# Optimization experiments

Measured on AMD Instinct MI355X. Metric: run time of the kernel, lower is better.

## Reference

```python
import jax, jax.numpy as jnp
import numpy as np

B, T, I, H, L, O = 256, 256, 512, 1024, 2, 5


def setup_inputs() -> dict:
    key = jax.random.key(0)
    ks = jax.random.split(key, 8)
    x = jax.random.normal(ks[0], (B, T, I), dtype=jnp.float32)
    hidden = jnp.zeros((L, 2, B, H), dtype=jnp.float32)  # [layer, (h,c), B, H]
    # per-layer stacked gate weights: [4(gates f,i,g,o), H, in+H]
    W0 = jax.random.normal(ks[1], (4, H, I + H), dtype=jnp.float32) * 0.01
    b0 = jnp.zeros((4, H), dtype=jnp.float32)
    W1 = jax.random.normal(ks[2], (4, H, H + H), dtype=jnp.float32) * 0.01
    b1 = jnp.zeros((4, H), dtype=jnp.float32)
    W_out = jax.random.normal(ks[3], (O, H), dtype=jnp.float32) * 0.01
    b_out = jnp.zeros((O,), dtype=jnp.float32)
    return {"x": x, "hidden": hidden, "W0": W0, "b0": b0,
            "W1": W1, "b1": b1, "W_out": W_out, "b_out": b_out}


def _lstm_cell(W, b):
    # W: [4, H, in+H], gates in order (f, i, g, o) matching the torch module
    def cell(carry, x_t):
        h, c = carry
        combined = jnp.concatenate([h, x_t], axis=1)        # [B, H+in]
        gates = jnp.einsum('bk,ghk->gbh', combined, W) + b[:, None, :]
        f = jax.nn.sigmoid(gates[0])
        i = jax.nn.sigmoid(gates[1])
        g = jnp.tanh(gates[2])
        o = jax.nn.sigmoid(gates[3])
        c_new = f * c + i * g
        h_new = o * jnp.tanh(c_new)
        return (h_new, c_new), h_new
    return cell


def reference(x, hidden, W0, b0, W1, b1, W_out, b_out):
    xs = jnp.swapaxes(x, 0, 1)  # [T, B, I]
    finals = []
    for layer, (W, b) in enumerate([(W0, b0), (W1, b1)]):
        h0, c0 = hidden[layer, 0], hidden[layer, 1]
        (hT, cT), ys = jax.lax.scan(_lstm_cell(W, b), (h0, c0), xs)
        xs = ys                      # feed this layer's h sequence to next layer
        finals.append(jnp.stack([hT, cT]))
    last_hidden = xs[-1]             # [B, H], last timestep of top layer
    output = last_hidden @ W_out.T + b_out
    return output, jnp.stack(finals)  # ([B,O], [L,2,B,H])
```

## Files before the change

kernel.cpp:

```cpp
#include <hip/hip_runtime.h>
#include <hip/hip_bf16.h>
#include <cstdint>
#include <cstddef>

#define Bdim 256
#define Tdim 256
#define Idim 512
#define Hdim 1024
#define Odim 5
#define BH (Bdim * Hdim)

using short8 = __attribute__((ext_vector_type(8))) short;
using f32x4  = __attribute__((ext_vector_type(4))) float;
typedef unsigned long long u64;

__device__ __forceinline__ short bf16_of(float f) {
  unsigned u = __builtin_bit_cast(unsigned, f);
  u += 0x7fffu + ((u >> 16) & 1u);
  return (short)(u >> 16);
}

__device__ __forceinline__ float sigmf(float x) {
  return 1.0f / (1.0f + __expf(-x));
}

__global__ __launch_bounds__(256) void k_init(const float* __restrict__ hidden,
    short* __restrict__ h0s0, short* __restrict__ h1s0) {
  int i = blockIdx.x * 256 + threadIdx.x;
  if (i < BH) {
    h0s0[i] = bf16_of(hidden[i]);
    h1s0[i] = bf16_of(hidden[2 * BH + i]);
  }
}

__device__ __forceinline__ void ctr_arrive(unsigned* ctr, int c) {
  __builtin_amdgcn_sched_barrier(0);
  __syncthreads();
  if (threadIdx.x == 0)
    __hip_atomic_fetch_add(&ctr[c * 32], 1u, __ATOMIC_RELAXED,
                           __HIP_MEMORY_SCOPE_AGENT);
}

__device__ __forceinline__ void ctr_poll2(unsigned* ctr, unsigned tg0, unsigned tg1) {
  if (threadIdx.x < 64) {
    const int lane = threadIdx.x;
    const unsigned tgt = (lane < 8) ? tg0 : (lane < 16 ? tg1 : 0u);
    unsigned* p = ctr + (lane < 16 ? lane : 0) * 32;
    for (;;) {
      bool ok = true;
      if (tgt) {
        unsigned v = __hip_atomic_load(p, __ATOMIC_RELAXED, __HIP_MEMORY_SCOPE_AGENT);
        ok = (v >= tgt);
      }
      if (__all(ok)) break;
      __builtin_amdgcn_s_sleep(1);
    }
  }
}

#define GEMM_H(A0P, A1P, K0, NBLK)                                             \
  for (int blk = 0; blk < (NBLK); ++blk) {                                     \
    short8 Ar0[8], Ar1[8], Br0[8], Br1[8];                                     \
    const int kb = (K0) + blk * 256 + kl;                                      \
    _Pragma("unroll")                                                          \
    for (int u = 0; u < 8; ++u) {                                              \
      const int k = kb + u * 32;                                               \
      Ar0[u] = *(const short8*)((A0P) + k);                                    \
      Ar1[u] = *(const short8*)((A1P) + k);                                    \
      Br0[u] = *(const short8*)(lb0 + k);                                      \
      Br1[u] = *(const short8*)(lb1 + k);                                      \
    }                                                                          \
    _Pragma("unroll")                                                          \
    for (int u = 0; u < 8; ++u) {                                              \
      acc[0][0] = __builtin_amdgcn_mfma_f32_16x16x32_bf16(Ar0[u], Br0[u], acc[0][0], 0, 0, 0); \
      acc[1][0] = __builtin_amdgcn_mfma_f32_16x16x32_bf16(Ar1[u], Br0[u], acc[1][0], 0, 0, 0); \
      acc[0][1] = __builtin_amdgcn_mfma_f32_16x16x32_bf16(Ar0[u], Br1[u], acc[0][1], 0, 0, 0); \
      acc[1][1] = __builtin_amdgcn_mfma_f32_16x16x32_bf16(Ar1[u], Br1[u], acc[1][1], 0, 0, 0); \
    }                                                                          \
  }

#define GEMM_X(XF0, XF1)                                                       \
  for (int blk = 0; blk < 4; ++blk) {                                          \
    f32x4 U0[4][2], U1[4][2]; short8 Bx0[4], Bx1[4];                           \
    const int kb = Hdim + blk * 128 + kl;                                      \
    _Pragma("unroll")                                                          \
    for (int u = 0; u < 4; ++u) {                                              \
      const int k = kb + u * 32;                                               \
      U0[u][0] = *(const f32x4*)((XF0) + k);                                   \
      U0[u][1] = *(const f32x4*)((XF0) + k + 4);                               \
      U1[u][0] = *(const f32x4*)((XF1) + k);                                   \
      U1[u][1] = *(const f32x4*)((XF1) + k + 4);                               \
      Bx0[u] = *(const short8*)(lb0 + k);                                      \
      Bx1[u] = *(const short8*)(lb1 + k);                                      \
    }                                                                          \
    _Pragma("unroll")                                                          \
    for (int u = 0; u < 4; ++u) {                                              \
      short8 a0 = {bf16_of(U0[u][0][0]), bf16_of(U0[u][0][1]), bf16_of(U0[u][0][2]), bf16_of(U0[u][0][3]), \
                   bf16_of(U0[u][1][0]), bf16_of(U0[u][1][1]), bf16_of(U0[u][1][2]), bf16_of(U0[u][1][3])}; \
      short8 a1 = {bf16_of(U1[u][0][0]), bf16_of(U1[u][0][1]), bf16_of(U1[u][0][2]), bf16_of(U1[u][0][3]), \
                   bf16_of(U1[u][1][0]), bf16_of(U1[u][1][1]), bf16_of(U1[u][1][2]), bf16_of(U1[u][1][3])}; \
      acc[0][0] = __builtin_amdgcn_mfma_f32_16x16x32_bf16(a0, Bx0[u], acc[0][0], 0, 0, 0); \
      acc[1][0] = __builtin_amdgcn_mfma_f32_16x16x32_bf16(a1, Bx0[u], acc[1][0], 0, 0, 0); \
      acc[0][1] = __builtin_amdgcn_mfma_f32_16x16x32_bf16(a0, Bx1[u], acc[0][1], 0, 0, 0); \
      acc[1][1] = __builtin_amdgcn_mfma_f32_16x16x32_bf16(a1, Bx1[u], acc[1][1], 0, 0, 0); \
    }                                                                          \
  }

__global__ __launch_bounds__(512, 1) void k_persist(
    const float* __restrict__ W0, const float* __restrict__ b0v,
    const float* __restrict__ W1, const float* __restrict__ b1v,
    const float* __restrict__ hidden,
    const float* __restrict__ x,
    short* __restrict__ h0seq,
    short* __restrict__ h1seq,
    float* __restrict__ finals,
    unsigned* __restrict__ ctr, int D) {
  extern __shared__ short lw[];
  const int tid  = threadIdx.x;
  const int wg   = blockIdx.x;
  const bool isL0 = (wg < 128);
  const int slot  = isL0 ? wg : wg - 128;
  const int hcol0 = slot * 8;
  const int K     = isL0 ? (Hdim + Idim) : (2 * Hdim);
  const int pitch = K + 8;
  const int layer = isL0 ? 0 : 1;
  const int myc   = layer * 8 + (wg & 7);
  const int lead  = D - 4;
  const float* Wsrc = isL0 ? W0 : W1;
  const float* bsrc = isL0 ? b0v : b1v;

  for (int r = 0; r < 32; ++r) {
    const float* src = Wsrc + (size_t)((r >> 3) * Hdim + hcol0 + (r & 7)) * K;
    short* dst = lw + r * pitch;
    for (int k = tid; k < K; k += 512) dst[k] = bf16_of(src[k]);
  }

  const int lane = tid & 63;
  const int wv   = tid >> 6;
  const int col  = lane & 15;
  const int rg   = lane >> 4;
  const int kl   = rg * 8;
  const int row0 = wv * 32 + col;

  float biasv[2];
  #pragma unroll
  for (int n = 0; n < 2; ++n)
    biasv[n] = bsrc[(n * 2 + (col >= 8 ? 1 : 0)) * Hdim + hcol0 + (col & 7)];

  float creg[2][4], hfin[2][4];
  #pragma unroll
  for (int m = 0; m < 2; ++m)
    #pragma unroll
    for (int j = 0; j < 4; ++j) {
      int b = wv * 32 + m * 16 + rg * 4 + j;
      creg[m][j] = hidden[(layer * 2 + 1) * BH + b * Hdim + hcol0 + (col & 7)];
      hfin[m][j] = 0.f;
    }

  if (tid == 0)
    (void)__hip_atomic_load(ctr, __ATOMIC_ACQUIRE, __HIP_MEMORY_SCOPE_AGENT);
  __syncthreads();

  const short* lb0 = lw + col * pitch;
  const short* lb1 = lw + (16 + col) * pitch;

  int i_cur = 0;
  for (int r = 0; r < 256; ++r) {
    const int i_next = (i_cur + 1 == D) ? 0 : i_cur + 1;
    f32x4 acc[2][2] = {};
    short* hout;

    if (isL0) {
      const float* xf0 = x + (size_t)(row0 * Tdim + r) * Idim - Hdim;
      const float* xf1 = x + (size_t)((row0 + 16) * Tdim + r) * Idim - Hdim;
      GEMM_X(xf0, xf1)
      __builtin_amdgcn_sched_barrier(0);
      unsigned tg1 = (r > lead) ? 16u * (unsigned)(r - lead) : 0u;
      if (r > 0 || tg1) ctr_poll2(ctr, 16u * (unsigned)r, tg1);
      if (tid == 0 && D < 257 && r >= D - 1)
        (void)__hip_atomic_load(ctr, __ATOMIC_ACQUIRE, __HIP_MEMORY_SCOPE_AGENT);
      __syncthreads();
      const short* Ah = h0seq + (size_t)i_cur * BH + row0 * Hdim;
      GEMM_H(Ah, Ah + 16 * Hdim, 0, 4)
      hout = h0seq + (size_t)i_next * BH;
    } else {
      ctr_poll2(ctr, 16u * (unsigned)(r + 1), 16u * (unsigned)r);
      if (tid == 0 && D < 257 && r >= D - 1)
        (void)__hip_atomic_load(ctr, __ATOMIC_ACQUIRE, __HIP_MEMORY_SCOPE_AGENT);
      __syncthreads();
      const short* Ax = h0seq + (size_t)i_next * BH + row0 * Hdim - Hdim;
      GEMM_H(Ax, Ax + 16 * Hdim, Hdim, 4)
      const short* Ah = h1seq + (size_t)i_cur * BH + row0 * Hdim;
      GEMM_H(Ah, Ah + 16 * Hdim, 0, 4)
      hout = h1seq + (size_t)i_next * BH;
    }

    #pragma unroll
    for (int m = 0; m < 2; ++m) {
      #pragma unroll
      for (int j = 0; j < 4; ++j) {
        float fi  = acc[m][0][j] + biasv[0];
        float go  = acc[m][1][j] + biasv[1];
        float iv_ = __shfl_xor(fi, 8, 64);
        float ov_ = __shfl_xor(go, 8, 64);
        float fv = sigmf(fi), iv = sigmf(iv_);
        float gv = tanhf(go), ov = sigmf(ov_);
        float cn = fv * creg[m][j] + iv * gv;
        creg[m][j] = cn;
        float hn = ov * tanhf(cn);
        hfin[m][j] = hn;
        unsigned hv = (unsigned)(unsigned short)bf16_of(hn);
        unsigned p1 = hv | ((unsigned)__shfl_xor((int)hv, 1, 64) << 16);
        u64 p2 = (u64)p1 | ((u64)(unsigned)__shfl_xor((int)p1, 2, 64) << 32);
        if ((col & 3) == 0 && col < 8) {
          int b = wv * 32 + m * 16 + rg * 4 + j;
          __hip_atomic_store((u64*)(hout + b * Hdim + hcol0 + col), p2,
                             __ATOMIC_RELAXED, __HIP_MEMORY_SCOPE_AGENT);
        }
      }
    }
    ctr_arrive(ctr, myc);
    i_cur = i_next;
  }

  if (col < 8) {
    #pragma unroll
    for (int m = 0; m < 2; ++m)
      #pragma unroll
      for (int j = 0; j < 4; ++j) {
        int b = wv * 32 + m * 16 + rg * 4 + j;
        finals[(layer * 2 + 0) * BH + b * Hdim + hcol0 + col] = hfin[m][j];
        finals[(layer * 2 + 1) * BH + b * Hdim + hcol0 + col] = creg[m][j];
      }
  }
}

__global__ __launch_bounds__(256) void k_outproj(const float* __restrict__ h1f,
    const float* __restrict__ Wout, const float* __restrict__ bout,
    float* __restrict__ out) {
  int b = blockIdx.x;
  int tid = threadIdx.x;
  float hv[4];
  #pragma unroll
  for (int j = 0; j < 4; ++j) hv[j] = h1f[b * Hdim + tid + j * 256];
  __shared__ float red[Odim][4];
  #pragma unroll
  for (int o = 0; o < Odim; ++o) {
    float p = 0.f;
    #pragma unroll
    for (int j = 0; j < 4; ++j) p += hv[j] * Wout[o * Hdim + tid + j * 256];
    #pragma unroll
    for (int s = 32; s > 0; s >>= 1) p += __shfl_down(p, s, 64);
    if ((tid & 63) == 0) red[o][tid >> 6] = p;
  }
  __syncthreads();
  if (tid < Odim)
    out[b * Odim + tid] = red[tid][0] + red[tid][1] + red[tid][2] + red[tid][3] + bout[tid];
}

extern "C" void kernel_launch(void* const* d_in, const int* in_sizes, int n_in,
                              void* d_out, int out_size, void* d_ws, size_t ws_size,
                              hipStream_t stream) {
  const float* x      = (const float*)d_in[0];
  const float* hidden = (const float*)d_in[1];
  const float* W0     = (const float*)d_in[2];
  const float* b0     = (const float*)d_in[3];
  const float* W1     = (const float*)d_in[4];
  const float* b1     = (const float*)d_in[5];
  const float* Wout   = (const float*)d_in[6];
  const float* bout   = (const float*)d_in[7];
  float* out = (float*)d_out;
  float* finals = out + Bdim * Odim;

  char* ws = (char*)d_ws;
  size_t off = 0;
  auto alloc = [&](size_t bytes) {
    void* p = ws + off;
    off += (bytes + 255) & ~(size_t)255;
    return p;
  };
  unsigned* ctr = (unsigned*)alloc(16 * 32 * sizeof(unsigned));
  const size_t seqSlotBytes = (size_t)BH * 2;
  size_t avail = (ws_size > off) ? (ws_size - off - 512) : 0;
  int D = (int)(avail / (2 * seqSlotBytes));
  if (D > 257) D = 257;
  if (D < 8) D = 8;
  short* h0seq = (short*)alloc((size_t)D * seqSlotBytes);
  short* h1seq = (short*)alloc((size_t)D * seqSlotBytes);

  k_init<<<BH / 256, 256, 0, stream>>>(hidden, h0seq, h1seq);
  hipMemsetAsync(ctr, 0, 16 * 32 * sizeof(unsigned), stream);

  const int ldsBytes = 32 * (2 * Hdim + 8) * 2;
  hipFuncSetAttribute((const void*)k_persist,
                      hipFuncAttributeMaxDynamicSharedMemorySize, ldsBytes);
  void* args[] = {(void*)&W0, (void*)&b0, (void*)&W1, (void*)&b1,
                  (void*)&hidden, (void*)&x,
                  (void*)&h0seq, (void*)&h1seq,
                  (void*)&finals, (void*)&ctr, (void*)&D};
  hipLaunchCooperativeKernel((const void*)k_persist, dim3(256), dim3(512),
                             args, ldsBytes, stream);

  k_outproj<<<Bdim, 256, 0, stream>>>(finals + 2 * BH, Wout, bout, out);
}
```

Measured before the change: 8.249 ms.

## Pre-convert x to bf16, double-buffer GEMM loads, reorder layer-1 waits

A new pre-pass converts x to bf16 in a [T,B,I] layout, so the layer-0 input GEMM inside the recurrent loop reads half the bytes and skips per-step conversion. The H-GEMM now uses two register sets so one block's loads overlap the previous block's MFMAs. Layer 1 first computes its own recurrent term and only then waits for layer 0's output for the step, which shortens the critical path between layers. The ring-buffer lead and acquire conditions are also adjusted. In exchange the code needs an extra workspace buffer and a conversion kernel, and carries more registers per thread.

```diff
diff --git a/kernel.cpp b/kernel.cpp
--- a/kernel.cpp
+++ b/kernel.cpp
@@ -22,6 +22,19 @@
 
 __device__ __forceinline__ float sigmf(float x) {
   return 1.0f / (1.0f + __expf(-x));
+}
+
+__global__ __launch_bounds__(256) void k_cvt_x(const float* __restrict__ src,
+                                               short* __restrict__ dst) {
+  int e = (blockIdx.x * 256 + threadIdx.x) * 8;
+  int row = e >> 9;
+  int i0  = e & 511;
+  int b = row >> 8, t = row & 255;
+  float4 u = *reinterpret_cast<const float4*>(src + e);
+  float4 v = *reinterpret_cast<const float4*>(src + e + 4);
+  short8 o = {bf16_of(u.x), bf16_of(u.y), bf16_of(u.z), bf16_of(u.w),
+              bf16_of(v.x), bf16_of(v.y), bf16_of(v.z), bf16_of(v.w)};
+  *reinterpret_cast<short8*>(dst + (((t << 8) + b) << 9) + i0) = o;
 }
 
 __global__ __launch_bounds__(256) void k_init(const float* __restrict__ hidden,
@@ -58,26 +71,34 @@
   }
 }
 
-#define GEMM_H(A0P, A1P, K0, NBLK)                                             \
-  for (int blk = 0; blk < (NBLK); ++blk) {                                     \
-    short8 Ar0[8], Ar1[8], Br0[8], Br1[8];                                     \
-    const int kb = (K0) + blk * 256 + kl;                                      \
-    _Pragma("unroll")                                                          \
+#define LOADBLK(SUF, A0P, A1P, KB)                                             \
+  { _Pragma("unroll")                                                          \
     for (int u = 0; u < 8; ++u) {                                              \
-      const int k = kb + u * 32;                                               \
-      Ar0[u] = *(const short8*)((A0P) + k);                                    \
-      Ar1[u] = *(const short8*)((A1P) + k);                                    \
-      Br0[u] = *(const short8*)(lb0 + k);                                      \
-      Br1[u] = *(const short8*)(lb1 + k);                                      \
-    }                                                                          \
-    _Pragma("unroll")                                                          \
+      const int k = (KB) + u * 32 + kl;                                        \
+      Ar0##SUF[u] = *(const short8*)((A0P) + k);                               \
+      Ar1##SUF[u] = *(const short8*)((A1P) + k);                               \
+      Br0##SUF[u] = *(const short8*)(lb0 + k);                                 \
+      Br1##SUF[u] = *(const short8*)(lb1 + k);                                 \
+    } }
+
+#define MFMABLK(SUF)                                                           \
+  { _Pragma("unroll")                                                          \
     for (int u = 0; u < 8; ++u) {                                              \
-      acc[0][0] = __builtin_amdgcn_mfma_f32_16x16x32_bf16(Ar0[u], Br0[u], acc[0][0], 0, 0, 0); \
-      acc[1][0] = __builtin_amdgcn_mfma_f32_16x16x32_bf16(Ar1[u], Br0[u], acc[1][0], 0, 0, 0); \
-      acc[0][1] = __builtin_amdgcn_mfma_f32_16x16x32_bf16(Ar0[u], Br1[u], acc[0][1], 0, 0, 0); \
-      acc[1][1] = __builtin_amdgcn_mfma_f32_16x16x32_bf16(Ar1[u], Br1[u], acc[1][1], 0, 0, 0); \
-    }                                                                          \
-  }
+      acc[0][0] = __builtin_amdgcn_mfma_f32_16x16x32_bf16(Ar0##SUF[u], Br0##SUF[u], acc[0][0], 0, 0, 0); \
+      acc[1][0] = __builtin_amdgcn_mfma_f32_16x16x32_bf16(Ar1##SUF[u], Br0##SUF[u], acc[1][0], 0, 0, 0); \
+      acc[0][1] = __builtin_amdgcn_mfma_f32_16x16x32_bf16(Ar0##SUF[u], Br1##SUF[u], acc[0][1], 0, 0, 0); \
+      acc[1][1] = __builtin_amdgcn_mfma_f32_16x16x32_bf16(Ar1##SUF[u], Br1##SUF[u], acc[1][1], 0, 0, 0); \
+    } }
+
+#define GEMM_SEG4(P0, P1, KB)                                                  \
+  LOADBLK(A, P0, P1, (KB))                                                     \
+  LOADBLK(B, P0, P1, (KB) + 256)                                               \
+  MFMABLK(A)                                                                   \
+  LOADBLK(A, P0, P1, (KB) + 512)                                               \
+  MFMABLK(B)                                                                   \
+  LOADBLK(B, P0, P1, (KB) + 768)                                               \
+  MFMABLK(A)                                                                   \
+  MFMABLK(B)
 
 #define GEMM_X(XF0, XF1)                                                       \
   for (int blk = 0; blk < 4; ++blk) {                                          \
@@ -110,7 +131,9 @@
     const float* __restrict__ W0, const float* __restrict__ b0v,
     const float* __restrict__ W1, const float* __restrict__ b1v,
     const float* __restrict__ hidden,
-    const float* __restrict__ x,
+    const float* __restrict__ xf,
+    const short* __restrict__ xbt,
+    int useXb,
     short* __restrict__ h0seq,
     short* __restrict__ h1seq,
     float* __restrict__ finals,
@@ -125,7 +148,7 @@
   const int pitch = K + 8;
   const int layer = isL0 ? 0 : 1;
   const int myc   = layer * 8 + (wg & 7);
-  const int lead  = D - 4;
+  const int lead  = (D > 4) ? (D - 2) : 2;
   const float* Wsrc = isL0 ? W0 : W1;
   const float* bsrc = isL0 ? b0v : b1v;
 
@@ -168,30 +191,44 @@
   for (int r = 0; r < 256; ++r) {
     const int i_next = (i_cur + 1 == D) ? 0 : i_cur + 1;
     f32x4 acc[2][2] = {};
+    short8 Ar0A[8], Ar1A[8], Br0A[8], Br1A[8];
+    short8 Ar0B[8], Ar1B[8], Br0B[8], Br1B[8];
     short* hout;
 
     if (isL0) {
-      const float* xf0 = x + (size_t)(row0 * Tdim + r) * Idim - Hdim;
-      const float* xf1 = x + (size_t)((row0 + 16) * Tdim + r) * Idim - Hdim;
-      GEMM_X(xf0, xf1)
+      if (useXb) {
+        const short* xa = xbt + (size_t)r * (Bdim * Idim) + row0 * Idim - Hdim;
+        const short* xc = xa + 16 * Idim;
+        LOADBLK(A, xa, xc, 1024)
+        LOADBLK(B, xa, xc, 1280)
+        MFMABLK(A)
+        MFMABLK(B)
+      } else {
+        const float* xf0 = xf + (size_t)(row0 * Tdim + r) * Idim - Hdim;
+        const float* xf1 = xf + (size_t)((row0 + 16) * Tdim + r) * Idim - Hdim;
+        GEMM_X(xf0, xf1)
+      }
       __builtin_amdgcn_sched_barrier(0);
       unsigned tg1 = (r > lead) ? 16u * (unsigned)(r - lead) : 0u;
       if (r > 0 || tg1) ctr_poll2(ctr, 16u * (unsigned)r, tg1);
-      if (tid == 0 && D < 257 && r >= D - 1)
+      if (tid == 0 && r > 0 && i_cur == 0)
         (void)__hip_atomic_load(ctr, __ATOMIC_ACQUIRE, __HIP_MEMORY_SCOPE_AGENT);
       __syncthreads();
-      const short* Ah = h0seq + (size_t)i_cur * BH + row0 * Hdim;
-      GEMM_H(Ah, Ah + 16 * Hdim, 0, 4)
+      const short* ah = h0seq + (size_t)i_cur * BH + row0 * Hdim;
+      GEMM_SEG4(ah, ah + 16 * Hdim, 0)
       hout = h0seq + (size_t)i_next * BH;
     } else {
-      ctr_poll2(ctr, 16u * (unsigned)(r + 1), 16u * (unsigned)r);
-      if (tid == 0 && D < 257 && r >= D - 1)
+      if (r > 0) ctr_poll2(ctr, 0u, 16u * (unsigned)r);
+      if (tid == 0 && r > 0 && i_cur == 0)
         (void)__hip_atomic_load(ctr, __ATOMIC_ACQUIRE, __HIP_MEMORY_SCOPE_AGENT);
       __syncthreads();
-      const short* Ax = h0seq + (size_t)i_next * BH + row0 * Hdim - Hdim;
-      GEMM_H(Ax, Ax + 16 * Hdim, Hdim, 4)
-      const short* Ah = h1seq + (size_t)i_cur * BH + row0 * Hdim;
-      GEMM_H(Ah, Ah + 16 * Hdim, 0, 4)
+      const short* ah = h1seq + (size_t)i_cur * BH + row0 * Hdim;
+      GEMM_SEG4(ah, ah + 16 * Hdim, 0)
+      __builtin_amdgcn_sched_barrier(0);
+      ctr_poll2(ctr, 16u * (unsigned)(r + 1), 0u);
+      __syncthreads();
+      const short* ax = h0seq + (size_t)i_next * BH + row0 * Hdim - Hdim;
+      GEMM_SEG4(ax, ax + 16 * Hdim, 1024)
       hout = h1seq + (size_t)i_next * BH;
     }
 
@@ -280,14 +317,23 @@
     return p;
   };
   unsigned* ctr = (unsigned*)alloc(16 * 32 * sizeof(unsigned));
-  const size_t seqSlotBytes = (size_t)BH * 2;
-  size_t avail = (ws_size > off) ? (ws_size - off - 512) : 0;
-  int D = (int)(avail / (2 * seqSlotBytes));
+  const size_t seqSlot = (size_t)BH * 2;
+  const size_t xbBytes = (size_t)Tdim * Bdim * Idim * 2;
+  int useXb = 0;
+  short* xbt = nullptr;
+  if (ws_size > off + xbBytes + 8 * 2 * seqSlot + (1 << 20)) {
+    useXb = 1;
+    xbt = (short*)alloc(xbBytes);
+  }
+  size_t avail = (ws_size > off + 512) ? (ws_size - off - 512) : 0;
+  int D = (int)(avail / (2 * seqSlot));
   if (D > 257) D = 257;
-  if (D < 8) D = 8;
-  short* h0seq = (short*)alloc((size_t)D * seqSlotBytes);
-  short* h1seq = (short*)alloc((size_t)D * seqSlotBytes);
-
+  if (D < 4) D = 4;
+  short* h0seq = (short*)alloc((size_t)D * seqSlot);
+  short* h1seq = (short*)alloc((size_t)D * seqSlot);
+
+  if (useXb)
+    k_cvt_x<<<(Tdim * Bdim * Idim) / (256 * 8), 256, 0, stream>>>(x, xbt);
   k_init<<<BH / 256, 256, 0, stream>>>(hidden, h0seq, h1seq);
   hipMemsetAsync(ctr, 0, 16 * 32 * sizeof(unsigned), stream);
 
@@ -295,7 +341,7 @@
   hipFuncSetAttribute((const void*)k_persist,
                       hipFuncAttributeMaxDynamicSharedMemorySize, ldsBytes);
   void* args[] = {(void*)&W0, (void*)&b0, (void*)&W1, (void*)&b1,
-                  (void*)&hidden, (void*)&x,
+                  (void*)&hidden, (void*)&x, (void*)&xbt, (void*)&useXb,
                   (void*)&h0seq, (void*)&h1seq,
                   (void*)&finals, (void*)&ctr, (void*)&D};
   hipLaunchCooperativeKernel((const void*)k_persist, dim3(256), dim3(512),
```

New measurement: 8.399 ms. Within noise of the previous version (+1.8%).
